# Optimization experiments

Hardware: AMD Instinct MI355X
Metric: run time of the kernel (lower is better)

The kernel has to match this reference:

```python
import jax, jax.numpy as jnp
import numpy as np

N = 50000      # nodes
E = 800000     # edges
IN = 128       # raw node feature dim
EMB = 64       # gene/pathway embedding dim
H = 256        # hidden dim
R = 12         # relations
B = 8          # num_bases (hardcoded in HRAN)
HEADS = 4      # attention heads (hardcoded)
NG = 20000     # n_gene
NPATH = 2000   # n_path
IN1 = IN + EMB # conv1 input dim


def _glorot(k, shape):
    fan_in, fan_out = shape[-2], shape[-1]
    s = np.sqrt(2.0 / (fan_in + fan_out)).astype(np.float32)
    return jax.random.normal(k, shape, jnp.float32) * s


def setup_inputs() -> dict:
    key = jax.random.key(0)
    ks = jax.random.split(key, 20)
    return {
        "x": jax.random.normal(ks[0], (N, IN), jnp.float32),
        "edge_index": jax.random.randint(ks[1], (2, E), 0, N),
        "edge_type": jax.random.randint(ks[2], (E,), 0, R),
        "gene_idx": jnp.arange(NG),
        "path_idx": jnp.arange(NPATH) + NG,  # disjoint from gene_idx
        "gene_emb": jax.random.normal(ks[3], (NG, EMB), jnp.float32) * 0.02,
        "path_emb": jax.random.normal(ks[4], (NPATH, EMB), jnp.float32) * 0.02,
        "comp1": _glorot(ks[5], (R, B)),
        "basis1": _glorot(ks[6], (B, IN1, H)),
        "root1": _glorot(ks[7], (IN1, H)),
        "bias1": jnp.zeros((H,), jnp.float32),
        "att1": _glorot(ks[8], (HEADS, H // HEADS)),
        "comp2": _glorot(ks[9], (R, B)),
        "basis2": _glorot(ks[10], (B, H, H)),
        "root2": _glorot(ks[11], (H, H)),
        "bias2": jnp.zeros((H,), jnp.float32),
        "att2": _glorot(ks[12], (HEADS, H // HEADS)),
        "pred_w": _glorot(ks[13], (H, 12)),
        "pred_b": jnp.zeros((12,), jnp.float32),
    }


def _rgcn(x, src, dst, et, comp, basis, root, bias):
    # Basis-decomposed RGCN with per-relation mean aggregation (PyG default).
    flat = dst * R + et                                   # combined (node, rel) id
    cnt = jax.ops.segment_sum(jnp.ones((src.shape[0],), jnp.float32), flat,
                              num_segments=N * R)
    w = 1.0 / jnp.maximum(cnt[flat], 1.0)                 # [E] mean normalizer
    coeff = comp[et] * w[:, None]                         # [E, B]
    xs = x[src]                                           # [E, in]  gather
    # aggregate in input space, then one dense contraction with the bases
    agg = jnp.stack([jax.ops.segment_sum(coeff[:, b, None] * xs, dst,
                                         num_segments=N)
                     for b in range(B)], axis=1)          # [N, B, in]
    return jnp.einsum('nbi,bio->no', agg, basis) + x @ root + bias


def _hran_conv(x, src, dst, et, comp, basis, root, bias, att):
    h = _rgcn(x, src, dst, et, comp, basis, root, bias)
    h = h.reshape(N, HEADS, -1)                           # [N, heads, hd]
    alpha = jax.nn.softmax((h * att).sum(-1), axis=1)     # softmax over heads
    return (h * alpha[..., None]).reshape(N, -1)


def reference(x, edge_index, edge_type, gene_idx, path_idx,
              gene_emb, path_emb,
              comp1, basis1, root1, bias1, att1,
              comp2, basis2, root2, bias2, att2,
              pred_w, pred_b):
    src, dst = edge_index[0], edge_index[1]
    x0 = jnp.concatenate([x, jnp.zeros((N, EMB), x.dtype)], axis=1)
    x0 = x0.at[gene_idx, IN:].add(gene_emb)
    x0 = x0.at[path_idx, IN:].add(path_emb)
    h = _hran_conv(x0, src, dst, edge_type, comp1, basis1, root1, bias1, att1)
    h = _hran_conv(h, src, dst, edge_type, comp2, basis2, root2, bias2, att2)
    return h @ pred_w + pred_b                            # [N, 12]
```

## Files before the change

### kernel.cpp

```cpp
#include <hip/hip_runtime.h>
#include <cstddef>

#define NN     50000
#define NE     800000
#define IND    128
#define EMBD   64
#define IN1    192
#define HDIM   256
#define RR     12
#define BB     8
#define NGENE  20000
#define NPATH  2000
#define NRK    (RR * NN)
#define SCB    1024
#define NSB    ((NRK + SCB - 1) / SCB)
#define CH0    25088

typedef __attribute__((ext_vector_type(8))) short short8;
typedef __attribute__((ext_vector_type(4))) float f32x4;
typedef unsigned short ushortT;
typedef __attribute__((address_space(3))) void lds_void;
typedef __attribute__((address_space(1))) const void glb_void;

__device__ __forceinline__ float bu2f(unsigned short u) {
  unsigned int x = ((unsigned int)u) << 16;
  return __builtin_bit_cast(float, x);
}
__device__ __forceinline__ unsigned short f2bu(float f) {
  unsigned int x = __builtin_bit_cast(unsigned int, f);
  unsigned int r = (x + 0x7fffu + ((x >> 16) & 1u)) >> 16;
  return (unsigned short)r;
}


__global__ void k_build_x0(const float* __restrict__ x, ushortT* __restrict__ x0) {
  int t = blockIdx.x * 256 + threadIdx.x;
  if (t >= NN * IN1) return;
  int n = t / IN1, i = t - n * IN1;
  float v = (i < IND) ? x[(size_t)n * IND + i] : 0.0f;
  int kt = i >> 6, ch = (i >> 3) & 7, off = i & 7;
  x0[(size_t)n * IN1 + kt * 64 + ((ch ^ (n & 7)) * 8) + off] = f2bu(v);
}

__global__ void k_add_emb(const int* __restrict__ idx, const float* __restrict__ emb,
                          ushortT* __restrict__ x0, int count) {
  int t = blockIdx.x * 256 + threadIdx.x;
  if (t >= count * EMBD) return;
  int g = t / EMBD, j = t - g * EMBD;
  int n = idx[g];
  int ch = (j >> 3) & 7, off = j & 7;
  x0[(size_t)n * IN1 + 128 + ((ch ^ (n & 7)) * 8) + off] = f2bu(emb[t]);
}

__global__ void k_count(const int* __restrict__ ei, const int* __restrict__ et,
                        int* __restrict__ cnt) {
  int e = blockIdx.x * 256 + threadIdx.x;
  if (e >= NE) return;
  atomicAdd(&cnt[ei[NE + e] * RR + et[e]], 1);
}

__global__ __launch_bounds__(256) void k_scan1(const int* __restrict__ cnt,
                                               int* __restrict__ bsum) {
  __shared__ int lds[256];
  int t = threadIdx.x;
  int base = blockIdx.x * SCB + t * 4;
  int s = 0;
#pragma unroll
  for (int j = 0; j < 4; j++) { int idx = base + j; if (idx < NRK) s += cnt[idx]; }
  lds[t] = s; __syncthreads();
  for (int d = 128; d > 0; d >>= 1) { if (t < d) lds[t] += lds[t + d]; __syncthreads(); }
  if (t == 0) bsum[blockIdx.x] = lds[0];
}

__global__ __launch_bounds__(1024) void k_scan2(const int* __restrict__ bsum,
                                                int* __restrict__ bscan) {
  __shared__ int lds[1024];
  int t = threadIdx.x;
  int v = (t < NSB) ? bsum[t] : 0;
  lds[t] = v; __syncthreads();
  for (int d = 1; d < 1024; d <<= 1) {
    int add = (t >= d) ? lds[t - d] : 0; __syncthreads();
    lds[t] += add; __syncthreads();
  }
  if (t < NSB) bscan[t] = lds[t] - v;
}

__global__ __launch_bounds__(256) void k_scan3(const int* __restrict__ cnt,
                                               const int* __restrict__ bscan,
                                               int* __restrict__ off) {
  __shared__ int lds[256];
  int t = threadIdx.x;
  int base = blockIdx.x * SCB + t * 4;
  int v[4]; int s = 0;
#pragma unroll
  for (int j = 0; j < 4; j++) { int idx = base + j; v[j] = (idx < NRK) ? cnt[idx] : 0; s += v[j]; }
  lds[t] = s; __syncthreads();
  for (int d = 1; d < 256; d <<= 1) {
    int add = (t >= d) ? lds[t - d] : 0; __syncthreads();
    lds[t] += add; __syncthreads();
  }
  int ex = lds[t] - s + bscan[blockIdx.x];
#pragma unroll
  for (int j = 0; j < 4; j++) {
    int idx = base + j;
    if (idx < NRK) { off[idx] = ex; ex += v[j]; }
  }
}

__global__ void k_fill(const int* __restrict__ ei, const int* __restrict__ et,
                       const int* __restrict__ off, int* __restrict__ fill,
                       int* __restrict__ srcs) {
  int e = blockIdx.x * 256 + threadIdx.x;
  if (e >= NE) return;
  int key = ei[NE + e] * RR + et[e];
  int pos = off[key] + atomicAdd(&fill[key], 1);
  srcs[pos] = ei[e];
}

__global__ void k_wbasis(const float* __restrict__ basis, ushortT* __restrict__ W,
                         int in_dim) {
  int t = blockIdx.x * 256 + threadIdx.x;
  int total = BB * HDIM * in_dim;
  if (t >= total) return;
  int i = t % in_dim;
  int o = (t / in_dim) & 255;
  int b = t / (in_dim * 256);
  W[t] = f2bu(basis[((size_t)b * in_dim + i) * HDIM + o]);
}

__global__ void k_troot(const float* __restrict__ root, ushortT* __restrict__ rt,
                        int in_dim) {
  int t = blockIdx.x * 256 + threadIdx.x;
  if (t >= in_dim * HDIM) return;
  int i = t % in_dim, o = t / in_dim;
  rt[t] = f2bu(root[(size_t)i * HDIM + o]);
}

__global__ __launch_bounds__(256) void k_aggb(const int* __restrict__ srcs,
                                              const int* __restrict__ off,
                                              const int* __restrict__ cnt,
                                              const float* __restrict__ comp,
                                              const ushortT* __restrict__ xin,
                                              ushortT* __restrict__ aggB,
                                              int in_dim, int row0, int nrows) {
  int wv = threadIdx.x >> 6;
  int lane = threadIdx.x & 63;
  int li = blockIdx.x * 4 + wv;
  if (li >= nrows) return;
  int dst = row0 + li;
  bool act = lane * 4 < in_dim;
  int kt = lane >> 4, chl = (lane >> 1) & 7, offh = (lane & 1) * 4;
  int kbase = kt * 64 + offh;

  auto gaddr = [&](int s) {
    return (const ushort4*)(xin + (size_t)s * in_dim + kbase + ((chl ^ (s & 7)) * 8));
  };

  int beg[RR], n[RR];
#pragma unroll
  for (int rl = 0; rl < RR; rl++) {
    beg[rl] = off[dst * RR + rl];
    n[rl]   = cnt[dst * RR + rl];
  }

  int sa[RR], sb[RR];
#pragma unroll
  for (int rl = 0; rl < RR; rl++) {
    sa[rl] = (n[rl] > 0) ? srcs[beg[rl]] : 0;
    sb[rl] = (n[rl] > 1) ? srcs[beg[rl] + 1] : 0;
  }

  ushort4 va[RR], vb[RR];
  if (act) {
#pragma unroll
    for (int rl = 0; rl < RR; rl++) va[rl] = *gaddr(sa[rl]);
#pragma unroll
    for (int rl = 0; rl < RR; rl++) vb[rl] = *gaddr(sb[rl]);
  }

  float acc[BB][4];
#pragma unroll
  for (int b = 0; b < BB; b++)
#pragma unroll
    for (int e = 0; e < 4; e++) acc[b][e] = 0.f;

#pragma unroll
  for (int rl = 0; rl < RR; rl++) {
    int ne = n[rl];
    if (ne == 0) continue;
    float s0 = 0.f, s1 = 0.f, s2 = 0.f, s3 = 0.f;
    if (act) {
      s0 = bu2f(va[rl].x); s1 = bu2f(va[rl].y); s2 = bu2f(va[rl].z); s3 = bu2f(va[rl].w);
      if (ne > 1) {
        s0 += bu2f(vb[rl].x); s1 += bu2f(vb[rl].y);
        s2 += bu2f(vb[rl].z); s3 += bu2f(vb[rl].w);
      }
    }
    for (int p = 2; p < ne; p++) {
      int s = srcs[beg[rl] + p];
      if (act) {
        ushort4 v = *gaddr(s);
        s0 += bu2f(v.x); s1 += bu2f(v.y); s2 += bu2f(v.z); s3 += bu2f(v.w);
      }
    }
    float wn = 1.0f / (float)ne;
#pragma unroll
    for (int b = 0; b < BB; b++) {
      float cb = comp[rl * BB + b] * wn;
      acc[b][0] += cb * s0; acc[b][1] += cb * s1;
      acc[b][2] += cb * s2; acc[b][3] += cb * s3;
    }
  }

  if (act) {
    size_t base = (size_t)li * BB * in_dim;
    int swz = (chl ^ (dst & 7)) * 8;
#pragma unroll
    for (int b = 0; b < BB; b++) {
      ushort4 o;
      o.x = f2bu(acc[b][0]); o.y = f2bu(acc[b][1]);
      o.z = f2bu(acc[b][2]); o.w = f2bu(acc[b][3]);
      *(ushort4*)(aggB + base + (size_t)b * in_dim + kbase + swz) = o;
    }
  }
}

__global__ __launch_bounds__(256, 2) void k_gemm(const ushortT* __restrict__ xin,
                                                 const ushortT* __restrict__ aggB,
                                                 const ushortT* __restrict__ W,
                                                 const float* __restrict__ bias,
                                                 const float* __restrict__ att,
                                                 ushortT* __restrict__ hout,
                                                 int in_dim, int row0, int row1) {
  __shared__ ushortT As[4][64 * 64];
  __shared__ float sm[64][4];
  const int tid = threadIdx.x;
  const int bm = row0 + blockIdx.x * 64;
  const int wv = tid >> 6, l = tid & 63;
  const int wc = wv;
  const int lm = l & 15, lq = l >> 4;
  const int nkt = in_dim >> 6;
  const int totKt = 9 * nkt;

  f32x4 acc[4][4];
#pragma unroll
  for (int mt = 0; mt < 4; mt++)
#pragma unroll
    for (int nt = 0; nt < 4; nt++) acc[mt][nt] = (f32x4){0.f, 0.f, 0.f, 0.f};

  struct WF { short8 f[2][4]; };
  WF w0, w1;

  auto stage = [&](int buf, int seg, int kt) {
#pragma unroll
    for (int j = 0; j < 2; j++) {
      int r = wv * 16 + j * 8;
      int g = bm + r + (l >> 3); if (g >= row1) g = row1 - 1;
      const ushortT* gp;
      if (seg == 0) gp = xin + (size_t)g * in_dim + kt * 64 + (l & 7) * 8;
      else gp = aggB + ((size_t)(g - row0) * 8 + (seg - 1)) * in_dim + kt * 64 + (l & 7) * 8;
      ushortT* lp = &As[buf][r * 64];
      __builtin_amdgcn_global_load_lds((glb_void*)gp, (lds_void*)lp, 16, 0, 0);
    }
  };

  auto loadW = [&](WF& wd, int seg, int kt) {
    const ushortT* wt = W + (size_t)(wc * 64 + lm) * in_dim +
                        (size_t)seg * 256 * in_dim + kt * 64 + lq * 8;
#pragma unroll
    for (int nt = 0; nt < 4; nt++) {
      wd.f[0][nt] = *(const short8*)(wt + (size_t)nt * 16 * in_dim);
      wd.f[1][nt] = *(const short8*)(wt + (size_t)nt * 16 * in_dim + 32);
    }
  };

  auto mfmaT = [&](int buf, const WF& wf) {
#pragma unroll
    for (int ks = 0; ks < 2; ks++) {
      short8 af[4];
#pragma unroll
      for (int mt = 0; mt < 4; mt++) {
        int ar = mt * 16 + lm;
        af[mt] = *(const short8*)(&As[buf][ar * 64 + (((ks * 4) + lq) ^ (ar & 7)) * 8]);
      }
#pragma unroll
      for (int mt = 0; mt < 4; mt++)
#pragma unroll
        for (int nt = 0; nt < 4; nt++)
          acc[mt][nt] = __builtin_amdgcn_mfma_f32_16x16x32_bf16(af[mt], wf.f[ks][nt],
                                                                acc[mt][nt], 0, 0, 0);
    }
  };

  int segS = 0, ktS = 0;
  int segW = 0, ktW = 0;
  auto bumpC = [&](int& s, int& k) {
    if (++k == nkt) { k = 0; if (++s == 9) { s = 8; k = nkt - 1; } }
  };

  auto body = [&](int t, WF& wuse, WF& wload) {
    loadW(wload, segW, ktW); bumpC(segW, ktW);
    asm volatile("s_waitcnt vmcnt(10)" ::: "memory");
    __builtin_amdgcn_s_barrier();
    __builtin_amdgcn_sched_barrier(0);
    stage((t + 3) & 3, segS, ktS); bumpC(segS, ktS);
    mfmaT(t & 3, wuse);
  };

  stage(0, segS, ktS); bumpC(segS, ktS);
  stage(1, segS, ktS); bumpC(segS, ktS);
  stage(2, segS, ktS); bumpC(segS, ktS);
  loadW(w0, segW, ktW); bumpC(segW, ktW);

  int t = 0;
  for (; t + 1 < totKt; t += 2) {
    body(t, w0, w1);
    body(t + 1, w1, w0);
  }
  if (t < totKt) body(t, w0, w1);
  asm volatile("s_waitcnt vmcnt(0)" ::: "memory");
  __syncthreads();

  float bv[4];
#pragma unroll
  for (int nt = 0; nt < 4; nt++) bv[nt] = bias[wc * 64 + nt * 16 + lm];
#pragma unroll
  for (int mt = 0; mt < 4; mt++)
#pragma unroll
    for (int nt = 0; nt < 4; nt++)
#pragma unroll
      for (int r = 0; r < 4; r++) acc[mt][nt][r] += bv[nt];

  float av[4];
#pragma unroll
  for (int nt = 0; nt < 4; nt++) av[nt] = att[wc * 64 + nt * 16 + lm];
#pragma unroll
  for (int mt = 0; mt < 4; mt++) {
    float sr[4];
#pragma unroll
    for (int r = 0; r < 4; r++)
      sr[r] = acc[mt][0][r] * av[0] + acc[mt][1][r] * av[1] +
              acc[mt][2][r] * av[2] + acc[mt][3][r] * av[3];
#pragma unroll
    for (int o = 1; o <= 8; o <<= 1) {
#pragma unroll
      for (int r = 0; r < 4; r++) sr[r] += __shfl_xor(sr[r], o, 64);
    }
    if (lm == 0) {
#pragma unroll
      for (int r = 0; r < 4; r++) sm[mt * 16 + lq * 4 + r][wc] = sr[r];
    }
  }
  __syncthreads();
  if (tid < 64) {
    float s0 = sm[tid][0], s1 = sm[tid][1], s2 = sm[tid][2], s3 = sm[tid][3];
    float mx = fmaxf(fmaxf(s0, s1), fmaxf(s2, s3));
    float e0 = __expf(s0 - mx), e1 = __expf(s1 - mx), e2 = __expf(s2 - mx), e3 = __expf(s3 - mx);
    float inv = 1.0f / (e0 + e1 + e2 + e3);
    sm[tid][0] = e0 * inv; sm[tid][1] = e1 * inv; sm[tid][2] = e2 * inv; sm[tid][3] = e3 * inv;
  }
  __syncthreads();
#pragma unroll
  for (int mt = 0; mt < 4; mt++) {
#pragma unroll
    for (int r = 0; r < 4; r++) {
      int rl = mt * 16 + lq * 4 + r;
      int row = bm + rl;
      if (row >= row1) continue;
      float al = sm[rl][wc];
      ushortT* op = hout + (size_t)row * HDIM + wc * 64;
      int key = row & 7;
#pragma unroll
      for (int nt = 0; nt < 4; nt++) {
        int ci = nt * 16 + lm;
        op[(((ci >> 3) ^ key) * 8) + (ci & 7)] = f2bu(acc[mt][nt][r] * al);
      }
    }
  }
}

__global__ void k_pred(const ushortT* __restrict__ h, const float* __restrict__ w,
                       const float* __restrict__ b, float* __restrict__ out) {
  int t = blockIdx.x * 256 + threadIdx.x;
  if (t >= NN * 12) return;
  int n = t / 12, j = t - n * 12;
  float acc = b[j];
  const ushortT* hp = h + (size_t)n * HDIM;
  int key = n & 7;
#pragma unroll
  for (int kt = 0; kt < 4; kt++)
#pragma unroll
    for (int cs = 0; cs < 8; cs++) {
      int ch = cs ^ key;
      int kb = kt * 64 + ch * 8;
      const ushortT* hh = hp + kt * 64 + cs * 8;
#pragma unroll
      for (int o = 0; o < 8; o++) acc += bu2f(hh[o]) * w[(kb + o) * 12 + j];
    }
  out[t] = acc;
}

extern "C" void kernel_launch(void* const* d_in, const int* in_sizes, int n_in,
                              void* d_out, int out_size, void* d_ws, size_t ws_size,
                              hipStream_t stream) {
  const float* x         = (const float*)d_in[0];
  const int*   edge_idx  = (const int*)d_in[1];
  const int*   edge_type = (const int*)d_in[2];
  const int*   gene_idx  = (const int*)d_in[3];
  const int*   path_idx  = (const int*)d_in[4];
  const float* gene_emb  = (const float*)d_in[5];
  const float* path_emb  = (const float*)d_in[6];
  const float* comp1     = (const float*)d_in[7];
  const float* basis1    = (const float*)d_in[8];
  const float* root1     = (const float*)d_in[9];
  const float* bias1     = (const float*)d_in[10];
  const float* att1      = (const float*)d_in[11];
  const float* comp2     = (const float*)d_in[12];
  const float* basis2    = (const float*)d_in[13];
  const float* root2     = (const float*)d_in[14];
  const float* bias2     = (const float*)d_in[15];
  const float* att2      = (const float*)d_in[16];
  const float* pred_w    = (const float*)d_in[17];
  const float* pred_b    = (const float*)d_in[18];
  float* out = (float*)d_out;

  char* ws = (char*)d_ws;
  ushortT* x0b   = (ushortT*)(ws);
  ushortT* h2b   = (ushortT*)(ws);
  ushortT* h1b   = (ushortT*)(ws + 25600000);
  ushortT* aggB  = (ushortT*)(ws + 51200000);
  ushortT* Wb1   = (ushortT*)(ws + 154000000);
  ushortT* Wb2   = (ushortT*)(ws + 155000000);
  int*     cnt   = (int*)(ws + 156200000);
  int*     off   = (int*)(ws + 158600000);
  int*     srcs  = (int*)(ws + 161000000);
  int*     fill  = (int*)(ws + 164200000);
  int*     bsum  = (int*)(ws + 166600000);
  int*     bscan = (int*)(ws + 166608000);

  dim3 blk(256);

  k_build_x0<<<dim3((NN * IN1) / 256), blk, 0, stream>>>(x, x0b);
  k_add_emb<<<dim3((NGENE * EMBD) / 256), blk, 0, stream>>>(gene_idx, gene_emb, x0b, NGENE);
  k_add_emb<<<dim3((NPATH * EMBD) / 256), blk, 0, stream>>>(path_idx, path_emb, x0b, NPATH);
  hipMemsetAsync(cnt, 0, NRK * 4, stream);
  hipMemsetAsync(fill, 0, NRK * 4, stream);
  k_count<<<dim3(NE / 256), blk, 0, stream>>>(edge_idx, edge_type, cnt);
  k_scan1<<<dim3(NSB), blk, 0, stream>>>(cnt, bsum);
  k_scan2<<<dim3(1), dim3(1024), 0, stream>>>(bsum, bscan);
  k_scan3<<<dim3(NSB), blk, 0, stream>>>(cnt, bscan, off);
  k_fill<<<dim3(NE / 256), blk, 0, stream>>>(edge_idx, edge_type, off, fill, srcs);
  k_troot<<<dim3((IN1 * HDIM) / 256), blk, 0, stream>>>(root1, Wb1, IN1);
  k_troot<<<dim3((HDIM * HDIM) / 256), blk, 0, stream>>>(root2, Wb2, HDIM);
  k_wbasis<<<dim3((BB * HDIM * IN1) / 256), blk, 0, stream>>>(basis1, Wb1 + 256 * IN1, IN1);
  k_wbasis<<<dim3((BB * HDIM * HDIM) / 256), blk, 0, stream>>>(basis2, Wb2 + 256 * HDIM, HDIM);

  const int r1 = CH0, n1 = CH0;
  const int n2 = NN - CH0;
  const int g1 = n1 / 64;
  const int g2 = (n2 + 63) / 64;

  k_aggb<<<dim3(n1 / 4), blk, 0, stream>>>(srcs, off, cnt, comp1, x0b, aggB, IN1, 0, n1);
  k_gemm<<<dim3(g1), blk, 0, stream>>>(x0b, aggB, Wb1, bias1, att1, h1b, IN1, 0, r1);
  k_aggb<<<dim3(n2 / 4), blk, 0, stream>>>(srcs, off, cnt, comp1, x0b, aggB, IN1, r1, n2);
  k_gemm<<<dim3(g2), blk, 0, stream>>>(x0b, aggB, Wb1, bias1, att1, h1b, IN1, r1, NN);

  k_aggb<<<dim3(n1 / 4), blk, 0, stream>>>(srcs, off, cnt, comp2, h1b, aggB, HDIM, 0, n1);
  k_gemm<<<dim3(g1), blk, 0, stream>>>(h1b, aggB, Wb2, bias2, att2, h2b, HDIM, 0, r1);
  k_aggb<<<dim3(n2 / 4), blk, 0, stream>>>(srcs, off, cnt, comp2, h1b, aggB, HDIM, r1, n2);
  k_gemm<<<dim3(g2), blk, 0, stream>>>(h1b, aggB, Wb2, bias2, att2, h2b, HDIM, r1, NN);

  k_pred<<<dim3((NN * 12 + 255) / 256), blk, 0, stream>>>(h2b, pred_w, pred_b, out);
}
```

Baseline: 791.0 us.

## Overlap chunked GEMM with next chunk's aggregation via fused heterogeneous launch

Result: slower. 915.4 us (+15.7%).

```diff
diff --git a/kernel.cpp b/kernel.cpp
--- a/kernel.cpp
+++ b/kernel.cpp
@@ -14,7 +14,9 @@
 #define NRK    (RR * NN)
 #define SCB    1024
 #define NSB    ((NRK + SCB - 1) / SCB)
-#define CH0    25088
+#define CHA    16704
+#define CHB    33408
+#define CH2N   (NN - CHB)
 
 typedef __attribute__((ext_vector_type(8))) short short8;
 typedef __attribute__((ext_vector_type(4))) float f32x4;
@@ -136,16 +138,15 @@
   rt[t] = f2bu(root[(size_t)i * HDIM + o]);
 }
 
-__global__ __launch_bounds__(256) void k_aggb(const int* __restrict__ srcs,
-                                              const int* __restrict__ off,
-                                              const int* __restrict__ cnt,
-                                              const float* __restrict__ comp,
-                                              const ushortT* __restrict__ xin,
-                                              ushortT* __restrict__ aggB,
-                                              int in_dim, int row0, int nrows) {
-  int wv = threadIdx.x >> 6;
-  int lane = threadIdx.x & 63;
-  int li = blockIdx.x * 4 + wv;
+
+__device__ __forceinline__ void dev_aggb(const int* __restrict__ srcs,
+                                         const int* __restrict__ off,
+                                         const int* __restrict__ cnt,
+                                         const float* __restrict__ comp,
+                                         const ushortT* __restrict__ xin,
+                                         ushortT* __restrict__ aggB,
+                                         int in_dim, int row0, int nrows,
+                                         int li, int lane) {
   if (li >= nrows) return;
   int dst = row0 + li;
   bool act = lane * 4 < in_dim;
@@ -225,6 +226,173 @@
   }
 }
 
+__device__ __forceinline__ void dev_gemm(ushortT* As , float (*sm)[4],
+                                         int gblk, int tid,
+                                         const ushortT* __restrict__ xin,
+                                         const ushortT* __restrict__ aggB,
+                                         const ushortT* __restrict__ W,
+                                         const float* __restrict__ bias,
+                                         const float* __restrict__ att,
+                                         ushortT* __restrict__ hout,
+                                         int in_dim, int row0, int row1) {
+  const int bm = row0 + gblk * 64;
+  const int wv = tid >> 6, l = tid & 63;
+  const int wc = wv;
+  const int lm = l & 15, lq = l >> 4;
+  const int nkt = in_dim >> 6;
+  const int totKt = 9 * nkt;
+
+  f32x4 acc[4][4];
+#pragma unroll
+  for (int mt = 0; mt < 4; mt++)
+#pragma unroll
+    for (int nt = 0; nt < 4; nt++) acc[mt][nt] = (f32x4){0.f, 0.f, 0.f, 0.f};
+
+  struct WF { short8 f[2][4]; };
+  WF w0, w1;
+
+  auto stage = [&](int buf, int seg, int kt) {
+#pragma unroll
+    for (int j = 0; j < 2; j++) {
+      int r = wv * 16 + j * 8;
+      int g = bm + r + (l >> 3); if (g >= row1) g = row1 - 1;
+      const ushortT* gp;
+      if (seg == 0) gp = xin + (size_t)g * in_dim + kt * 64 + (l & 7) * 8;
+      else gp = aggB + ((size_t)(g - row0) * 8 + (seg - 1)) * in_dim + kt * 64 + (l & 7) * 8;
+      ushortT* lp = &As[(size_t)buf * 64 * 64 + r * 64];
+      __builtin_amdgcn_global_load_lds((glb_void*)gp, (lds_void*)lp, 16, 0, 0);
+    }
+  };
+
+  auto loadW = [&](WF& wd, int seg, int kt) {
+    const ushortT* wt = W + (size_t)(wc * 64 + lm) * in_dim +
+                        (size_t)seg * 256 * in_dim + kt * 64 + lq * 8;
+#pragma unroll
+    for (int nt = 0; nt < 4; nt++) {
+      wd.f[0][nt] = *(const short8*)(wt + (size_t)nt * 16 * in_dim);
+      wd.f[1][nt] = *(const short8*)(wt + (size_t)nt * 16 * in_dim + 32);
+    }
+  };
+
+  auto mfmaT = [&](int buf, const WF& wf) {
+#pragma unroll
+    for (int ks = 0; ks < 2; ks++) {
+      short8 af[4];
+#pragma unroll
+      for (int mt = 0; mt < 4; mt++) {
+        int ar = mt * 16 + lm;
+        af[mt] = *(const short8*)(&As[(size_t)buf * 64 * 64 + ar * 64 +
+                                      (((ks * 4) + lq) ^ (ar & 7)) * 8]);
+      }
+#pragma unroll
+      for (int mt = 0; mt < 4; mt++)
+#pragma unroll
+        for (int nt = 0; nt < 4; nt++)
+          acc[mt][nt] = __builtin_amdgcn_mfma_f32_16x16x32_bf16(af[mt], wf.f[ks][nt],
+                                                                acc[mt][nt], 0, 0, 0);
+    }
+  };
+
+  int segS = 0, ktS = 0;
+  int segW = 0, ktW = 0;
+  auto bumpC = [&](int& s, int& k) {
+    if (++k == nkt) { k = 0; if (++s == 9) { s = 8; k = nkt - 1; } }
+  };
+
+  auto body = [&](int t, WF& wuse, WF& wload) {
+    loadW(wload, segW, ktW); bumpC(segW, ktW);
+    asm volatile("s_waitcnt vmcnt(10)" ::: "memory");
+    __builtin_amdgcn_s_barrier();
+    __builtin_amdgcn_sched_barrier(0);
+    stage((t + 3) & 3, segS, ktS); bumpC(segS, ktS);
+    mfmaT(t & 3, wuse);
+  };
+
+  stage(0, segS, ktS); bumpC(segS, ktS);
+  stage(1, segS, ktS); bumpC(segS, ktS);
+  stage(2, segS, ktS); bumpC(segS, ktS);
+  loadW(w0, segW, ktW); bumpC(segW, ktW);
+
+  int t = 0;
+  for (; t + 1 < totKt; t += 2) {
+    body(t, w0, w1);
+    body(t + 1, w1, w0);
+  }
+  if (t < totKt) body(t, w0, w1);
+  asm volatile("s_waitcnt vmcnt(0)" ::: "memory");
+  __syncthreads();
+
+  float bv[4];
+#pragma unroll
+  for (int nt = 0; nt < 4; nt++) bv[nt] = bias[wc * 64 + nt * 16 + lm];
+#pragma unroll
+  for (int mt = 0; mt < 4; mt++)
+#pragma unroll
+    for (int nt = 0; nt < 4; nt++)
+#pragma unroll
+      for (int r = 0; r < 4; r++) acc[mt][nt][r] += bv[nt];
+
+  float av[4];
+#pragma unroll
+  for (int nt = 0; nt < 4; nt++) av[nt] = att[wc * 64 + nt * 16 + lm];
+#pragma unroll
+  for (int mt = 0; mt < 4; mt++) {
+    float sr[4];
+#pragma unroll
+    for (int r = 0; r < 4; r++)
+      sr[r] = acc[mt][0][r] * av[0] + acc[mt][1][r] * av[1] +
+              acc[mt][2][r] * av[2] + acc[mt][3][r] * av[3];
+#pragma unroll
+    for (int o = 1; o <= 8; o <<= 1) {
+#pragma unroll
+      for (int r = 0; r < 4; r++) sr[r] += __shfl_xor(sr[r], o, 64);
+    }
+    if (lm == 0) {
+#pragma unroll
+      for (int r = 0; r < 4; r++) sm[mt * 16 + lq * 4 + r][wc] = sr[r];
+    }
+  }
+  __syncthreads();
+  if (tid < 64) {
+    float s0 = sm[tid][0], s1 = sm[tid][1], s2 = sm[tid][2], s3 = sm[tid][3];
+    float mx = fmaxf(fmaxf(s0, s1), fmaxf(s2, s3));
+    float e0 = __expf(s0 - mx), e1 = __expf(s1 - mx), e2 = __expf(s2 - mx), e3 = __expf(s3 - mx);
+    float inv = 1.0f / (e0 + e1 + e2 + e3);
+    sm[tid][0] = e0 * inv; sm[tid][1] = e1 * inv; sm[tid][2] = e2 * inv; sm[tid][3] = e3 * inv;
+  }
+  __syncthreads();
+#pragma unroll
+  for (int mt = 0; mt < 4; mt++) {
+#pragma unroll
+    for (int r = 0; r < 4; r++) {
+      int rl = mt * 16 + lq * 4 + r;
+      int row = bm + rl;
+      if (row >= row1) continue;
+      float al = sm[rl][wc];
+      ushortT* op = hout + (size_t)row * HDIM + wc * 64;
+      int key = row & 7;
+#pragma unroll
+      for (int nt = 0; nt < 4; nt++) {
+        int ci = nt * 16 + lm;
+        op[(((ci >> 3) ^ key) * 8) + (ci & 7)] = f2bu(acc[mt][nt][r] * al);
+      }
+    }
+  }
+}
+
+
+__global__ __launch_bounds__(256) void k_aggb(const int* __restrict__ srcs,
+                                              const int* __restrict__ off,
+                                              const int* __restrict__ cnt,
+                                              const float* __restrict__ comp,
+                                              const ushortT* __restrict__ xin,
+                                              ushortT* __restrict__ aggB,
+                                              int in_dim, int row0, int nrows) {
+  int wv = threadIdx.x >> 6, lane = threadIdx.x & 63;
+  dev_aggb(srcs, off, cnt, comp, xin, aggB, in_dim, row0, nrows,
+           blockIdx.x * 4 + wv, lane);
+}
+
 __global__ __launch_bounds__(256, 2) void k_gemm(const ushortT* __restrict__ xin,
                                                  const ushortT* __restrict__ aggB,
                                                  const ushortT* __restrict__ W,
@@ -234,148 +402,33 @@
                                                  int in_dim, int row0, int row1) {
   __shared__ ushortT As[4][64 * 64];
   __shared__ float sm[64][4];
-  const int tid = threadIdx.x;
-  const int bm = row0 + blockIdx.x * 64;
-  const int wv = tid >> 6, l = tid & 63;
-  const int wc = wv;
-  const int lm = l & 15, lq = l >> 4;
-  const int nkt = in_dim >> 6;
-  const int totKt = 9 * nkt;
-
-  f32x4 acc[4][4];
-#pragma unroll
-  for (int mt = 0; mt < 4; mt++)
-#pragma unroll
-    for (int nt = 0; nt < 4; nt++) acc[mt][nt] = (f32x4){0.f, 0.f, 0.f, 0.f};
-
-  struct WF { short8 f[2][4]; };
-  WF w0, w1;
-
-  auto stage = [&](int buf, int seg, int kt) {
-#pragma unroll
-    for (int j = 0; j < 2; j++) {
-      int r = wv * 16 + j * 8;
-      int g = bm + r + (l >> 3); if (g >= row1) g = row1 - 1;
-      const ushortT* gp;
-      if (seg == 0) gp = xin + (size_t)g * in_dim + kt * 64 + (l & 7) * 8;
-      else gp = aggB + ((size_t)(g - row0) * 8 + (seg - 1)) * in_dim + kt * 64 + (l & 7) * 8;
-      ushortT* lp = &As[buf][r * 64];
-      __builtin_amdgcn_global_load_lds((glb_void*)gp, (lds_void*)lp, 16, 0, 0);
-    }
-  };
-
-  auto loadW = [&](WF& wd, int seg, int kt) {
-    const ushortT* wt = W + (size_t)(wc * 64 + lm) * in_dim +
-                        (size_t)seg * 256 * in_dim + kt * 64 + lq * 8;
-#pragma unroll
-    for (int nt = 0; nt < 4; nt++) {
-      wd.f[0][nt] = *(const short8*)(wt + (size_t)nt * 16 * in_dim);
-      wd.f[1][nt] = *(const short8*)(wt + (size_t)nt * 16 * in_dim + 32);
-    }
-  };
-
-  auto mfmaT = [&](int buf, const WF& wf) {
-#pragma unroll
-    for (int ks = 0; ks < 2; ks++) {
-      short8 af[4];
-#pragma unroll
-      for (int mt = 0; mt < 4; mt++) {
-        int ar = mt * 16 + lm;
-        af[mt] = *(const short8*)(&As[buf][ar * 64 + (((ks * 4) + lq) ^ (ar & 7)) * 8]);
-      }
-#pragma unroll
-      for (int mt = 0; mt < 4; mt++)
-#pragma unroll
-        for (int nt = 0; nt < 4; nt++)
-          acc[mt][nt] = __builtin_amdgcn_mfma_f32_16x16x32_bf16(af[mt], wf.f[ks][nt],
-                                                                acc[mt][nt], 0, 0, 0);
-    }
-  };
-
-  int segS = 0, ktS = 0;
-  int segW = 0, ktW = 0;
-  auto bumpC = [&](int& s, int& k) {
-    if (++k == nkt) { k = 0; if (++s == 9) { s = 8; k = nkt - 1; } }
-  };
-
-  auto body = [&](int t, WF& wuse, WF& wload) {
-    loadW(wload, segW, ktW); bumpC(segW, ktW);
-    asm volatile("s_waitcnt vmcnt(10)" ::: "memory");
-    __builtin_amdgcn_s_barrier();
-    __builtin_amdgcn_sched_barrier(0);
-    stage((t + 3) & 3, segS, ktS); bumpC(segS, ktS);
-    mfmaT(t & 3, wuse);
-  };
-
-  stage(0, segS, ktS); bumpC(segS, ktS);
-  stage(1, segS, ktS); bumpC(segS, ktS);
-  stage(2, segS, ktS); bumpC(segS, ktS);
-  loadW(w0, segW, ktW); bumpC(segW, ktW);
-
-  int t = 0;
-  for (; t + 1 < totKt; t += 2) {
-    body(t, w0, w1);
-    body(t + 1, w1, w0);
-  }
-  if (t < totKt) body(t, w0, w1);
-  asm volatile("s_waitcnt vmcnt(0)" ::: "memory");
-  __syncthreads();
-
-  float bv[4];
-#pragma unroll
-  for (int nt = 0; nt < 4; nt++) bv[nt] = bias[wc * 64 + nt * 16 + lm];
-#pragma unroll
-  for (int mt = 0; mt < 4; mt++)
-#pragma unroll
-    for (int nt = 0; nt < 4; nt++)
-#pragma unroll
-      for (int r = 0; r < 4; r++) acc[mt][nt][r] += bv[nt];
-
-  float av[4];
-#pragma unroll
-  for (int nt = 0; nt < 4; nt++) av[nt] = att[wc * 64 + nt * 16 + lm];
-#pragma unroll
-  for (int mt = 0; mt < 4; mt++) {
-    float sr[4];
-#pragma unroll
-    for (int r = 0; r < 4; r++)
-      sr[r] = acc[mt][0][r] * av[0] + acc[mt][1][r] * av[1] +
-              acc[mt][2][r] * av[2] + acc[mt][3][r] * av[3];
-#pragma unroll
-    for (int o = 1; o <= 8; o <<= 1) {
-#pragma unroll
-      for (int r = 0; r < 4; r++) sr[r] += __shfl_xor(sr[r], o, 64);
-    }
-    if (lm == 0) {
-#pragma unroll
-      for (int r = 0; r < 4; r++) sm[mt * 16 + lq * 4 + r][wc] = sr[r];
-    }
-  }
-  __syncthreads();
-  if (tid < 64) {
-    float s0 = sm[tid][0], s1 = sm[tid][1], s2 = sm[tid][2], s3 = sm[tid][3];
-    float mx = fmaxf(fmaxf(s0, s1), fmaxf(s2, s3));
-    float e0 = __expf(s0 - mx), e1 = __expf(s1 - mx), e2 = __expf(s2 - mx), e3 = __expf(s3 - mx);
-    float inv = 1.0f / (e0 + e1 + e2 + e3);
-    sm[tid][0] = e0 * inv; sm[tid][1] = e1 * inv; sm[tid][2] = e2 * inv; sm[tid][3] = e3 * inv;
-  }
-  __syncthreads();
-#pragma unroll
-  for (int mt = 0; mt < 4; mt++) {
-#pragma unroll
-    for (int r = 0; r < 4; r++) {
-      int rl = mt * 16 + lq * 4 + r;
-      int row = bm + rl;
-      if (row >= row1) continue;
-      float al = sm[rl][wc];
-      ushortT* op = hout + (size_t)row * HDIM + wc * 64;
-      int key = row & 7;
-#pragma unroll
-      for (int nt = 0; nt < 4; nt++) {
-        int ci = nt * 16 + lm;
-        op[(((ci >> 3) ^ key) * 8) + (ci & 7)] = f2bu(acc[mt][nt][r] * al);
-      }
-    }
+  dev_gemm(&As[0][0], sm, blockIdx.x, threadIdx.x,
+           xin, aggB, W, bias, att, hout, in_dim, row0, row1);
+}
+
+__global__ __launch_bounds__(256, 2) void k_fused(const ushortT* __restrict__ xin,
+                                                  const ushortT* __restrict__ aggR,
+                                                  const ushortT* __restrict__ W,
+                                                  const float* __restrict__ bias,
+                                                  const float* __restrict__ att,
+                                                  ushortT* __restrict__ hout,
+                                                  int in_dim, int grow0, int grow1,
+                                                  int gB,
+                                                  const int* __restrict__ srcs,
+                                                  const int* __restrict__ off,
+                                                  const int* __restrict__ cnt,
+                                                  const float* __restrict__ comp,
+                                                  ushortT* __restrict__ aggW,
+                                                  int arow0, int anrows) {
+  __shared__ ushortT As[4][64 * 64];
+  __shared__ float sm[64][4];
+  if ((int)blockIdx.x < gB) {
+    dev_gemm(&As[0][0], sm, blockIdx.x, threadIdx.x,
+             xin, aggR, W, bias, att, hout, in_dim, grow0, grow1);
+  } else {
+    int wv = threadIdx.x >> 6, lane = threadIdx.x & 63;
+    dev_aggb(srcs, off, cnt, comp, xin, aggW, in_dim, arow0, anrows,
+             ((int)blockIdx.x - gB) * 4 + wv, lane);
   }
 }
 
@@ -428,15 +481,16 @@
   ushortT* x0b   = (ushortT*)(ws);
   ushortT* h2b   = (ushortT*)(ws);
   ushortT* h1b   = (ushortT*)(ws + 25600000);
-  ushortT* aggB  = (ushortT*)(ws + 51200000);
-  ushortT* Wb1   = (ushortT*)(ws + 154000000);
-  ushortT* Wb2   = (ushortT*)(ws + 155000000);
-  int*     cnt   = (int*)(ws + 156200000);
-  int*     off   = (int*)(ws + 158600000);
-  int*     srcs  = (int*)(ws + 161000000);
-  int*     fill  = (int*)(ws + 164200000);
-  int*     bsum  = (int*)(ws + 166600000);
-  int*     bscan = (int*)(ws + 166608000);
+  ushortT* aggB0 = (ushortT*)(ws + 51200000);
+  ushortT* aggB1 = (ushortT*)(ws + 119619584);
+  ushortT* Wb1   = (ushortT*)(ws + 188039168);
+  ushortT* Wb2   = (ushortT*)(ws + 188923904);
+  int*     cnt   = (int*)(ws + 190103552);
+  int*     off   = (int*)(ws + 192503552);
+  int*     srcs  = (int*)(ws + 194903552);
+  int*     fill  = (int*)(ws + 198103552);
+  int*     bsum  = (int*)(ws + 200503552);
+  int*     bscan = (int*)(ws + 200507648);
 
   dim3 blk(256);
 
@@ -455,20 +509,28 @@
   k_wbasis<<<dim3((BB * HDIM * IN1) / 256), blk, 0, stream>>>(basis1, Wb1 + 256 * IN1, IN1);
   k_wbasis<<<dim3((BB * HDIM * HDIM) / 256), blk, 0, stream>>>(basis2, Wb2 + 256 * HDIM, HDIM);
 
-  const int r1 = CH0, n1 = CH0;
-  const int n2 = NN - CH0;
-  const int g1 = n1 / 64;
-  const int g2 = (n2 + 63) / 64;
-
-  k_aggb<<<dim3(n1 / 4), blk, 0, stream>>>(srcs, off, cnt, comp1, x0b, aggB, IN1, 0, n1);
-  k_gemm<<<dim3(g1), blk, 0, stream>>>(x0b, aggB, Wb1, bias1, att1, h1b, IN1, 0, r1);
-  k_aggb<<<dim3(n2 / 4), blk, 0, stream>>>(srcs, off, cnt, comp1, x0b, aggB, IN1, r1, n2);
-  k_gemm<<<dim3(g2), blk, 0, stream>>>(x0b, aggB, Wb1, bias1, att1, h1b, IN1, r1, NN);
-
-  k_aggb<<<dim3(n1 / 4), blk, 0, stream>>>(srcs, off, cnt, comp2, h1b, aggB, HDIM, 0, n1);
-  k_gemm<<<dim3(g1), blk, 0, stream>>>(h1b, aggB, Wb2, bias2, att2, h2b, HDIM, 0, r1);
-  k_aggb<<<dim3(n2 / 4), blk, 0, stream>>>(srcs, off, cnt, comp2, h1b, aggB, HDIM, r1, n2);
-  k_gemm<<<dim3(g2), blk, 0, stream>>>(h1b, aggB, Wb2, bias2, att2, h2b, HDIM, r1, NN);
+  const int gB01 = CHA / 64;
+  const int gB2  = (CH2N + 63) / 64;
+  const int aB01 = CHA / 4;
+  const int aB2  = (CH2N + 3) / 4;
+
+  k_aggb<<<dim3(aB01), blk, 0, stream>>>(srcs, off, cnt, comp1, x0b, aggB0, IN1, 0, CHA);
+  k_fused<<<dim3(gB01 + aB01), blk, 0, stream>>>(x0b, aggB0, Wb1, bias1, att1, h1b,
+                                                 IN1, 0, CHA, gB01,
+                                                 srcs, off, cnt, comp1, aggB1, CHA, CHA);
+  k_fused<<<dim3(gB01 + aB2), blk, 0, stream>>>(x0b, aggB1, Wb1, bias1, att1, h1b,
+                                                IN1, CHA, CHB, gB01,
+                                                srcs, off, cnt, comp1, aggB0, CHB, CH2N);
+  k_gemm<<<dim3(gB2), blk, 0, stream>>>(x0b, aggB0, Wb1, bias1, att1, h1b, IN1, CHB, NN);
+
+  k_aggb<<<dim3(aB01), blk, 0, stream>>>(srcs, off, cnt, comp2, h1b, aggB0, HDIM, 0, CHA);
+  k_fused<<<dim3(gB01 + aB01), blk, 0, stream>>>(h1b, aggB0, Wb2, bias2, att2, h2b,
+                                                 HDIM, 0, CHA, gB01,
+                                                 srcs, off, cnt, comp2, aggB1, CHA, CHA);
+  k_fused<<<dim3(gB01 + aB2), blk, 0, stream>>>(h1b, aggB1, Wb2, bias2, att2, h2b,
+                                                HDIM, CHA, CHB, gB01,
+                                                srcs, off, cnt, comp2, aggB0, CHB, CH2N);
+  k_gemm<<<dim3(gB2), blk, 0, stream>>>(h1b, aggB0, Wb2, bias2, att2, h2b, HDIM, CHB, NN);
 
   k_pred<<<dim3((NN * 12 + 255) / 256), blk, 0, stream>>>(h2b, pred_w, pred_b, out);
 }
```
